# Performance work log

Hardware: AMD Instinct MI355X
Metric: run time of the kernel (lower is better)

Reference implementation:

```python
import jax, jax.numpy as jnp
import numpy as np

N_NODES = 50000
N_EDGES = 800000
IN_DIM = 128
OUT_DIM = 128
N_REL = 8


def setup_inputs() -> dict:
    key = jax.random.key(0)
    k1, k2, k3, k4, k5 = jax.random.split(key, 5)
    x = jax.random.normal(k1, (N_NODES, IN_DIM), dtype=jnp.float32)
    edge_index = jax.random.randint(k2, (2, N_EDGES), 0, N_NODES, dtype=jnp.int32).astype(jnp.int64)
    edge_type = jax.random.randint(k3, (N_EDGES,), 0, N_REL, dtype=jnp.int32).astype(jnp.int64)
    W = jax.random.normal(k4, (N_REL, IN_DIM, OUT_DIM), dtype=jnp.float32) * 0.02
    W0 = jax.random.normal(k5, (IN_DIM, OUT_DIM), dtype=jnp.float32) * 0.02
    return {"x": x, "edge_index": edge_index, "edge_type": edge_type,
            "num_nodes": N_NODES, "W": W, "W0": W0}


def reference(x, edge_index, edge_type, num_nodes, W, W0):
    src = edge_index[0]
    dst = edge_index[1]
    # Per-relation transform of ALL nodes, matching the original loop's x @ W[r].
    xW = jnp.einsum('nd,rdo->rno', x, W)            # [R, N, OUT]
    msgs = xW[edge_type, src]                       # [E, OUT] gather per edge
    agg = jax.ops.segment_sum(msgs, dst, num_segments=num_nodes)  # scatter-add to dst
    out = x @ W0 + agg                              # root/self term
    deg = jax.ops.segment_sum(jnp.ones_like(dst, dtype=out.dtype), dst,
                              num_segments=num_nodes)
    deg = jnp.maximum(deg, 1.0)
    return out / deg[:, None]
```

## Files before the change

kernel.cpp:

```cpp
#include <hip/hip_runtime.h>
#include <hip/hip_bf16.h>
#include <cstdint>
#include <cstddef>


#define NDIM 128
#define NREL 8
#define KCAT 1152
#define COARSE 196
#define EPB 4096

typedef __attribute__((ext_vector_type(8))) short bf16x8;
typedef __attribute__((ext_vector_type(4))) float f32x4;
typedef unsigned int uint32;

__device__ __forceinline__ short f2bf(float f){
  __hip_bfloat16 h = __float2bfloat16(f);
  return *reinterpret_cast<short*>(&h);
}
__device__ __forceinline__ float bfl(uint32 v){ return __uint_as_float(v << 16); }
__device__ __forceinline__ float bfh(uint32 v){ return __uint_as_float(v & 0xFFFF0000u); }

__device__ __forceinline__ void gload_lds16(const void* g, void* l){
  __builtin_amdgcn_global_load_lds(
      (const __attribute__((address_space(1))) unsigned int*)g,
      (__attribute__((address_space(3))) unsigned int*)l, 16, 0, 0);
}

__global__ void k_prep(const float* __restrict__ x, uint32* __restrict__ xb, int n4, int xblocks,
                       const float* __restrict__ W, const float* __restrict__ W0,
                       short* __restrict__ Wb, int wblocks,
                       const int* __restrict__ ei, int* flag, int* coarse_cnt){
  int b = blockIdx.x;
  if (b < xblocks){
    int i = b * 256 + threadIdx.x;
    if (i >= n4) return;
    float4 f = ((const float4*)x)[i];
    uint32 lo = ((uint32)(unsigned short)f2bf(f.x)) | (((uint32)(unsigned short)f2bf(f.y)) << 16);
    uint32 hi = ((uint32)(unsigned short)f2bf(f.z)) | (((uint32)(unsigned short)f2bf(f.w)) << 16);
    ((uint2*)xb)[i] = make_uint2(lo, hi);
  } else if (b < xblocks + wblocks){
    int i = (b - xblocks) * 256 + threadIdx.x;
    if (i >= NDIM * KCAT) return;
    int j  = i / KCAT;
    int t  = i - j * KCAT;
    int r  = t >> 7;
    int kd = t & 127;
    float v = (r < NREL) ? W[(((size_t)r * NDIM + kd) << 7) + j] : W0[((size_t)kd << 7) + j];
    Wb[i] = f2bf(v);
  } else {
    if (threadIdx.x < COARSE) coarse_cnt[threadIdx.x] = 0;
    if (threadIdx.x < 64){
      int v = ei[2 * threadIdx.x + 1];
      unsigned long long m = __ballot(v == 0);
      if (threadIdx.x == 0) flag[0] = (m == ~0ull) ? 1 : 0;
    }
  }
}

__global__ __launch_bounds__(1024) void k_hist(
    const int* __restrict__ ei, const int* __restrict__ et, const int* __restrict__ flag,
    uint32* __restrict__ kv, unsigned char* __restrict__ ctmp,
    int* __restrict__ coarse_cnt, int* __restrict__ blockRes, int E){
  __shared__ int h[COARSE];
  const int b = blockIdx.x;
  for (int i = threadIdx.x; i < COARSE; i += 1024) h[i] = 0;
  __syncthreads();
  const int is64 = flag[0];
  const int e0 = b * EPB;
  for (int i = threadIdx.x; i < EPB; i += 1024){
    int e = e0 + i;
    if (e < E){
      int s, d, t;
      if (is64){ s = ei[2*e]; d = ei[2*(E + e)]; t = et[2*e]; }
      else     { s = ei[e];   d = ei[E + e];     t = et[e];   }
      int c = d >> 8;
      kv[e]   = (uint32)s | ((uint32)t << 16) | ((uint32)(d & 255) << 19);
      ctmp[e] = (unsigned char)c;
      atomicAdd(&h[c], 1);
    }
  }
  __syncthreads();
  for (int c = threadIdx.x; c < COARSE; c += 1024){
    int cnt = h[c];
    int res = 0;
    if (cnt > 0) res = atomicAdd(&coarse_cnt[c], cnt);
    blockRes[b * COARSE + c] = res;
  }
}

__global__ void k_base(const int* __restrict__ coarse_cnt, int* __restrict__ base){
  __shared__ int sm[256];
  int t = threadIdx.x;
  int v = (t < COARSE) ? coarse_cnt[t] : 0;
  sm[t] = v; __syncthreads();
  #pragma unroll
  for (int off = 1; off < 256; off <<= 1){
    int xv = 0; if (t >= off) xv = sm[t - off];
    __syncthreads(); sm[t] += xv; __syncthreads();
  }
  if (t <= COARSE) base[t] = sm[t] - v;
}

__global__ __launch_bounds__(1024) void k_cscatter(
    const uint32* __restrict__ kv, const unsigned char* __restrict__ ctmp,
    const int* __restrict__ base, const int* __restrict__ blockRes,
    uint32* __restrict__ ckv, int E){
  __shared__ int cur[COARSE];
  const int b = blockIdx.x;
  for (int c = threadIdx.x; c < COARSE; c += 1024)
    cur[c] = base[c] + blockRes[b * COARSE + c];
  __syncthreads();
  const int e0 = b * EPB;
  for (int i = threadIdx.x; i < EPB; i += 1024){
    int e = e0 + i;
    if (e < E){
      uint32 v = kv[e];
      int c = ctmp[e];
      int pos = atomicAdd(&cur[c], 1);
      ckv[pos] = v;
    }
  }
}

__global__ __launch_bounds__(1024) void k_fine(
    const uint32* __restrict__ ckv, const int* __restrict__ base,
    uint32* __restrict__ esort, int* __restrict__ rs, int N){
  __shared__ int h[256];
  __shared__ int cur[256];
  const int c  = blockIdx.x;
  const int lo = base[c], hi = base[c + 1];
  const int t  = threadIdx.x;
  if (t < 256) h[t] = 0;
  __syncthreads();
  for (int i = lo + t; i < hi; i += 1024)
    atomicAdd(&h[(ckv[i] >> 19) & 255], 1);
  __syncthreads();
  int v = (t < 256) ? h[t] : 0;
  __syncthreads();
  for (int off = 1; off < 256; off <<= 1){
    int xv = 0;
    if (t < 256 && t >= off) xv = h[t - off];
    __syncthreads();
    if (t < 256) h[t] += xv;
    __syncthreads();
  }
  if (t < 256){
    int excl = h[t] - v;
    cur[t] = lo + excl;
    int idx = c * 256 + t;
    if (idx <= N) rs[idx] = lo + excl;
  }
  __syncthreads();
  for (int i = lo + t; i < hi; i += 1024){
    uint32 v2 = ckv[i];
    int pos = atomicAdd(&cur[(v2 >> 19) & 255], 1);
    esort[pos] = v2;
  }
}

__global__ __launch_bounds__(256) void k_agg(const uint32* __restrict__ xb,
                                             const int* __restrict__ rs,
                                             const uint32* __restrict__ esort,
                                             uint32* __restrict__ hcat,
                                             float* __restrict__ invdeg, int N){
  int wave = threadIdx.x >> 6;
  int lane = threadIdx.x & 63;
  int n = blockIdx.x * 4 + wave;
  if (n >= N) return;
  int beg = rs[n], end = rs[n + 1];
  float2 acc[NREL];
  #pragma unroll
  for (int r = 0; r < NREL; ++r){ acc[r].x = 0.f; acc[r].y = 0.f; }

  int i = beg;
  for (; i + 3 < end; i += 4){
    uint32 p0 = esort[i], p1 = esort[i+1], p2 = esort[i+2], p3 = esort[i+3];
    uint32 v0 = xb[(size_t)(p0 & 0xFFFF) * 64 + lane];
    uint32 v1 = xb[(size_t)(p1 & 0xFFFF) * 64 + lane];
    uint32 v2 = xb[(size_t)(p2 & 0xFFFF) * 64 + lane];
    uint32 v3 = xb[(size_t)(p3 & 0xFFFF) * 64 + lane];
    switch ((p0 >> 16) & 7){
      case 0: acc[0].x+=bfl(v0); acc[0].y+=bfh(v0); break; case 1: acc[1].x+=bfl(v0); acc[1].y+=bfh(v0); break;
      case 2: acc[2].x+=bfl(v0); acc[2].y+=bfh(v0); break; case 3: acc[3].x+=bfl(v0); acc[3].y+=bfh(v0); break;
      case 4: acc[4].x+=bfl(v0); acc[4].y+=bfh(v0); break; case 5: acc[5].x+=bfl(v0); acc[5].y+=bfh(v0); break;
      case 6: acc[6].x+=bfl(v0); acc[6].y+=bfh(v0); break; case 7: acc[7].x+=bfl(v0); acc[7].y+=bfh(v0); break;
    }
    switch ((p1 >> 16) & 7){
      case 0: acc[0].x+=bfl(v1); acc[0].y+=bfh(v1); break; case 1: acc[1].x+=bfl(v1); acc[1].y+=bfh(v1); break;
      case 2: acc[2].x+=bfl(v1); acc[2].y+=bfh(v1); break; case 3: acc[3].x+=bfl(v1); acc[3].y+=bfh(v1); break;
      case 4: acc[4].x+=bfl(v1); acc[4].y+=bfh(v1); break; case 5: acc[5].x+=bfl(v1); acc[5].y+=bfh(v1); break;
      case 6: acc[6].x+=bfl(v1); acc[6].y+=bfh(v1); break; case 7: acc[7].x+=bfl(v1); acc[7].y+=bfh(v1); break;
    }
    switch ((p2 >> 16) & 7){
      case 0: acc[0].x+=bfl(v2); acc[0].y+=bfh(v2); break; case 1: acc[1].x+=bfl(v2); acc[1].y+=bfh(v2); break;
      case 2: acc[2].x+=bfl(v2); acc[2].y+=bfh(v2); break; case 3: acc[3].x+=bfl(v2); acc[3].y+=bfh(v2); break;
      case 4: acc[4].x+=bfl(v2); acc[4].y+=bfh(v2); break; case 5: acc[5].x+=bfl(v2); acc[5].y+=bfh(v2); break;
      case 6: acc[6].x+=bfl(v2); acc[6].y+=bfh(v2); break; case 7: acc[7].x+=bfl(v2); acc[7].y+=bfh(v2); break;
    }
    switch ((p3 >> 16) & 7){
      case 0: acc[0].x+=bfl(v3); acc[0].y+=bfh(v3); break; case 1: acc[1].x+=bfl(v3); acc[1].y+=bfh(v3); break;
      case 2: acc[2].x+=bfl(v3); acc[2].y+=bfh(v3); break; case 3: acc[3].x+=bfl(v3); acc[3].y+=bfh(v3); break;
      case 4: acc[4].x+=bfl(v3); acc[4].y+=bfh(v3); break; case 5: acc[5].x+=bfl(v3); acc[5].y+=bfh(v3); break;
      case 6: acc[6].x+=bfl(v3); acc[6].y+=bfh(v3); break; case 7: acc[7].x+=bfl(v3); acc[7].y+=bfh(v3); break;
    }
  }
  for (; i < end; ++i){
    uint32 p = esort[i];
    uint32 v = xb[(size_t)(p & 0xFFFF) * 64 + lane];
    switch ((p >> 16) & 7){
      case 0: acc[0].x+=bfl(v); acc[0].y+=bfh(v); break; case 1: acc[1].x+=bfl(v); acc[1].y+=bfh(v); break;
      case 2: acc[2].x+=bfl(v); acc[2].y+=bfh(v); break; case 3: acc[3].x+=bfl(v); acc[3].y+=bfh(v); break;
      case 4: acc[4].x+=bfl(v); acc[4].y+=bfh(v); break; case 5: acc[5].x+=bfl(v); acc[5].y+=bfh(v); break;
      case 6: acc[6].x+=bfl(v); acc[6].y+=bfh(v); break; case 7: acc[7].x+=bfl(v); acc[7].y+=bfh(v); break;
    }
  }

  size_t b2 = (size_t)n * (KCAT / 2);
  #pragma unroll
  for (int r = 0; r < NREL; ++r){
    __hip_bfloat162 pk = __float22bfloat162_rn(make_float2(acc[r].x, acc[r].y));
    hcat[b2 + r * 64 + lane] = *reinterpret_cast<uint32*>(&pk);
  }
  hcat[b2 + 512 + lane] = xb[(size_t)n * 64 + lane];
  if (lane == 0){
    int d = end - beg;
    invdeg[n] = 1.0f / (float)(d > 0 ? d : 1);
  }
}

__global__ __launch_bounds__(256) void k_gemm2(
    const short* __restrict__ acat, const short* __restrict__ wb,
    const float* __restrict__ invdeg, float* __restrict__ out, int N)
{
  __shared__ char smem[49152];
  char* As0 = smem;
  char* As1 = smem + 8192;
  char* Bs0 = smem + 16384;
  char* Bs1 = smem + 32768;

  const int tid  = threadIdx.x;
  const int lane = tid & 63;
  const int wid  = tid >> 6;
  const int wr   = wid >> 1;
  const int wc   = wid & 1;
  const int n0   = blockIdx.x * 64;
  const int lr   = lane & 15;
  const int lq   = lane >> 4;

  f32x4 acc[2][4];
  #pragma unroll
  for (int m = 0; m < 2; ++m)
    #pragma unroll
    for (int p = 0; p < 4; ++p)
      acc[m][p] = (f32x4){0.f, 0.f, 0.f, 0.f};

  const int srow = tid >> 3;
  const int scs  = tid & 7;

  auto STAGE = [&](char* Ab, char* Bb, int ks){
    const short* ab = acat + (size_t)n0 * KCAT + ks * 64;
    #pragma unroll
    for (int q = 0; q < 2; ++q){
      int row = q * 32 + srow;
      const short* src = ab + (size_t)row * KCAT + ((scs ^ (row & 7)) << 3);
      gload_lds16(src, Ab + q * 4096 + (wid << 10));
    }
    const short* bb = wb + ks * 64;
    #pragma unroll
    for (int q = 0; q < 4; ++q){
      int j = q * 32 + srow;
      const short* src = bb + (size_t)j * KCAT + ((scs ^ (j & 7)) << 3);
      gload_lds16(src, Bb + q * 4096 + (wid << 10));
    }
  };

  auto COMPUTE = [&](const char* Ab, const char* Bb){
    bf16x8 a[2][2], b[2][4];
    #pragma unroll
    for (int kk = 0; kk < 2; ++kk){
      #pragma unroll
      for (int m = 0; m < 2; ++m){
        int row = wr * 32 + m * 16 + lr;
        int c   = kk * 4 + lq;
        a[kk][m] = *(const bf16x8*)(Ab + row * 128 + ((c ^ (row & 7)) << 4));
      }
      #pragma unroll
      for (int p = 0; p < 4; ++p){
        int j = wc * 64 + p * 16 + lr;
        int c = kk * 4 + lq;
        b[kk][p] = *(const bf16x8*)(Bb + j * 128 + ((c ^ (j & 7)) << 4));
      }
    }
    #pragma unroll
    for (int kk = 0; kk < 2; ++kk)
      #pragma unroll
      for (int m = 0; m < 2; ++m)
        #pragma unroll
        for (int p = 0; p < 4; ++p)
          acc[m][p] = __builtin_amdgcn_mfma_f32_16x16x32_bf16(a[kk][m], b[kk][p], acc[m][p], 0, 0, 0);
  };

  STAGE(As0, Bs0, 0);
  __syncthreads();
  for (int ks = 0; ks < 18; ks += 2){
    STAGE(As1, Bs1, ks + 1);
    COMPUTE(As0, Bs0);
    __syncthreads();
    if (ks + 2 < 18) STAGE(As0, Bs0, ks + 2);
    COMPUTE(As1, Bs1);
    __syncthreads();
  }

  #pragma unroll
  for (int m = 0; m < 2; ++m){
    int rbase = n0 + wr * 32 + m * 16 + lq * 4;
    #pragma unroll
    for (int v = 0; v < 4; ++v){
      int ro = rbase + v;
      if (ro < N){
        float inv = invdeg[ro];
        #pragma unroll
        for (int p = 0; p < 4; ++p)
          out[(((size_t)ro) << 7) + wc * 64 + p * 16 + lr] = acc[m][p][v] * inv;
      }
    }
  }
}

extern "C" void kernel_launch(void* const* d_in, const int* in_sizes, int n_in,
                              void* d_out, int out_size, void* d_ws, size_t ws_size,
                              hipStream_t stream){
  const float* x  = (const float*)d_in[0];
  const int*   ei = (const int*)d_in[1];
  const int*   et = (const int*)d_in[2];
  const float* W  = (const float*)d_in[4];
  const float* W0 = (const float*)d_in[5];
  float* out = (float*)d_out;

  const int N = in_sizes[0] / NDIM;
  const int E = in_sizes[2];
  const int Npad = N + 64;
  const int nblkE = (E + EPB - 1) / EPB;

  char* ws = (char*)d_ws;
  size_t off = 0;
  auto alloc = [&](size_t bytes)->size_t{
    size_t p = off; off = (off + bytes + 255) & ~(size_t)255; return p;
  };
  size_t o_flag = alloc(4);
  size_t o_kv   = alloc((size_t)E * 4);
  size_t o_ct   = alloc((size_t)E);
  size_t o_ckv  = alloc((size_t)E * 4);
  size_t o_es   = alloc((size_t)E * 4);
  size_t o_cc   = alloc(COARSE * 4);
  size_t o_base = alloc((COARSE + 2) * 4);
  size_t o_br   = alloc((size_t)nblkE * COARSE * 4);
  size_t o_rs   = alloc((size_t)(N + 1) * 4);
  size_t o_inv  = alloc((size_t)N * 4);
  size_t o_h    = alloc((size_t)Npad * KCAT * 2);
  size_t o_wb   = alloc((size_t)NDIM * KCAT * 2);
  size_t o_xb   = alloc((size_t)N * NDIM * 2);
  (void)ws_size;

  int*  flag   = (int*)(ws + o_flag);
  uint32* kv   = (uint32*)(ws + o_kv);
  unsigned char* ctmp = (unsigned char*)(ws + o_ct);
  uint32* ckv  = (uint32*)(ws + o_ckv);
  uint32* esort= (uint32*)(ws + o_es);
  int*  ccnt   = (int*)(ws + o_cc);
  int*  base   = (int*)(ws + o_base);
  int*  bres   = (int*)(ws + o_br);
  int*  rs     = (int*)(ws + o_rs);
  float* invdeg= (float*)(ws + o_inv);
  uint32* hcat = (uint32*)(ws + o_h);
  short* acat  = (short*)(ws + o_h);
  short* Wbs   = (short*)(ws + o_wb);
  uint32* xb   = (uint32*)(ws + o_xb);

  const int n4      = N * NDIM / 4;
  const int xblocks = (n4 + 255) / 256;
  const int wblocks = (NDIM * KCAT + 255) / 256;

  k_prep<<<xblocks + wblocks + 1, 256, 0, stream>>>(
      x, xb, n4, xblocks, W, W0, Wbs, wblocks, ei, flag, ccnt);
  k_hist<<<nblkE, 1024, 0, stream>>>(ei, et, flag, kv, ctmp, ccnt, bres, E);
  k_base<<<1, 256, 0, stream>>>(ccnt, base);
  k_cscatter<<<nblkE, 1024, 0, stream>>>(kv, ctmp, base, bres, ckv, E);
  k_fine<<<COARSE, 1024, 0, stream>>>(ckv, base, esort, rs, N);
  k_agg<<<(N + 3) / 4, 256, 0, stream>>>(xb, rs, esort, hcat, invdeg, N);
  k_gemm2<<<(N + 63) / 64, 256, 0, stream>>>(acat, Wbs, invdeg, out, N);
}
```

Measured before the change: 125.9 us.

## Load GEMM weights directly to registers, unroll gather by eight, use nontemporal stores

The GEMM kernel stops staging the weight tile through LDS. Each wave now loads its B fragments straight from global memory into registers, double-buffered across k-steps, which cuts shared memory from 48KB to 16KB and may raise occupancy. The cost is more global/L2 traffic, since waves sharing a column slice each fetch the same weights. The aggregation loop is unrolled by eight to keep more gathers in flight, and the hcat and output writes become nontemporal stores to avoid polluting the cache.

```diff
diff --git a/kernel.cpp b/kernel.cpp
--- a/kernel.cpp
+++ b/kernel.cpp
@@ -159,6 +159,14 @@
   }
 }
 
+#define ACCUM(P, V) \
+  switch (((P) >> 16) & 7){ \
+    case 0: acc[0].x+=bfl(V); acc[0].y+=bfh(V); break; case 1: acc[1].x+=bfl(V); acc[1].y+=bfh(V); break; \
+    case 2: acc[2].x+=bfl(V); acc[2].y+=bfh(V); break; case 3: acc[3].x+=bfl(V); acc[3].y+=bfh(V); break; \
+    case 4: acc[4].x+=bfl(V); acc[4].y+=bfh(V); break; case 5: acc[5].x+=bfl(V); acc[5].y+=bfh(V); break; \
+    case 6: acc[6].x+=bfl(V); acc[6].y+=bfh(V); break; case 7: acc[7].x+=bfl(V); acc[7].y+=bfh(V); break; \
+  }
+
 __global__ __launch_bounds__(256) void k_agg(const uint32* __restrict__ xb,
                                              const int* __restrict__ rs,
                                              const uint32* __restrict__ esort,
@@ -174,55 +182,41 @@
   for (int r = 0; r < NREL; ++r){ acc[r].x = 0.f; acc[r].y = 0.f; }
 
   int i = beg;
+  for (; i + 7 < end; i += 8){
+    uint32 p0 = esort[i],   p1 = esort[i+1], p2 = esort[i+2], p3 = esort[i+3];
+    uint32 p4 = esort[i+4], p5 = esort[i+5], p6 = esort[i+6], p7 = esort[i+7];
+    uint32 v0 = xb[(size_t)(p0 & 0xFFFF) * 64 + lane];
+    uint32 v1 = xb[(size_t)(p1 & 0xFFFF) * 64 + lane];
+    uint32 v2 = xb[(size_t)(p2 & 0xFFFF) * 64 + lane];
+    uint32 v3 = xb[(size_t)(p3 & 0xFFFF) * 64 + lane];
+    uint32 v4 = xb[(size_t)(p4 & 0xFFFF) * 64 + lane];
+    uint32 v5 = xb[(size_t)(p5 & 0xFFFF) * 64 + lane];
+    uint32 v6 = xb[(size_t)(p6 & 0xFFFF) * 64 + lane];
+    uint32 v7 = xb[(size_t)(p7 & 0xFFFF) * 64 + lane];
+    ACCUM(p0, v0) ACCUM(p1, v1) ACCUM(p2, v2) ACCUM(p3, v3)
+    ACCUM(p4, v4) ACCUM(p5, v5) ACCUM(p6, v6) ACCUM(p7, v7)
+  }
   for (; i + 3 < end; i += 4){
     uint32 p0 = esort[i], p1 = esort[i+1], p2 = esort[i+2], p3 = esort[i+3];
     uint32 v0 = xb[(size_t)(p0 & 0xFFFF) * 64 + lane];
     uint32 v1 = xb[(size_t)(p1 & 0xFFFF) * 64 + lane];
     uint32 v2 = xb[(size_t)(p2 & 0xFFFF) * 64 + lane];
     uint32 v3 = xb[(size_t)(p3 & 0xFFFF) * 64 + lane];
-    switch ((p0 >> 16) & 7){
-      case 0: acc[0].x+=bfl(v0); acc[0].y+=bfh(v0); break; case 1: acc[1].x+=bfl(v0); acc[1].y+=bfh(v0); break;
-      case 2: acc[2].x+=bfl(v0); acc[2].y+=bfh(v0); break; case 3: acc[3].x+=bfl(v0); acc[3].y+=bfh(v0); break;
-      case 4: acc[4].x+=bfl(v0); acc[4].y+=bfh(v0); break; case 5: acc[5].x+=bfl(v0); acc[5].y+=bfh(v0); break;
-      case 6: acc[6].x+=bfl(v0); acc[6].y+=bfh(v0); break; case 7: acc[7].x+=bfl(v0); acc[7].y+=bfh(v0); break;
-    }
-    switch ((p1 >> 16) & 7){
-      case 0: acc[0].x+=bfl(v1); acc[0].y+=bfh(v1); break; case 1: acc[1].x+=bfl(v1); acc[1].y+=bfh(v1); break;
-      case 2: acc[2].x+=bfl(v1); acc[2].y+=bfh(v1); break; case 3: acc[3].x+=bfl(v1); acc[3].y+=bfh(v1); break;
-      case 4: acc[4].x+=bfl(v1); acc[4].y+=bfh(v1); break; case 5: acc[5].x+=bfl(v1); acc[5].y+=bfh(v1); break;
-      case 6: acc[6].x+=bfl(v1); acc[6].y+=bfh(v1); break; case 7: acc[7].x+=bfl(v1); acc[7].y+=bfh(v1); break;
-    }
-    switch ((p2 >> 16) & 7){
-      case 0: acc[0].x+=bfl(v2); acc[0].y+=bfh(v2); break; case 1: acc[1].x+=bfl(v2); acc[1].y+=bfh(v2); break;
-      case 2: acc[2].x+=bfl(v2); acc[2].y+=bfh(v2); break; case 3: acc[3].x+=bfl(v2); acc[3].y+=bfh(v2); break;
-      case 4: acc[4].x+=bfl(v2); acc[4].y+=bfh(v2); break; case 5: acc[5].x+=bfl(v2); acc[5].y+=bfh(v2); break;
-      case 6: acc[6].x+=bfl(v2); acc[6].y+=bfh(v2); break; case 7: acc[7].x+=bfl(v2); acc[7].y+=bfh(v2); break;
-    }
-    switch ((p3 >> 16) & 7){
-      case 0: acc[0].x+=bfl(v3); acc[0].y+=bfh(v3); break; case 1: acc[1].x+=bfl(v3); acc[1].y+=bfh(v3); break;
-      case 2: acc[2].x+=bfl(v3); acc[2].y+=bfh(v3); break; case 3: acc[3].x+=bfl(v3); acc[3].y+=bfh(v3); break;
-      case 4: acc[4].x+=bfl(v3); acc[4].y+=bfh(v3); break; case 5: acc[5].x+=bfl(v3); acc[5].y+=bfh(v3); break;
-      case 6: acc[6].x+=bfl(v3); acc[6].y+=bfh(v3); break; case 7: acc[7].x+=bfl(v3); acc[7].y+=bfh(v3); break;
-    }
+    ACCUM(p0, v0) ACCUM(p1, v1) ACCUM(p2, v2) ACCUM(p3, v3)
   }
   for (; i < end; ++i){
     uint32 p = esort[i];
     uint32 v = xb[(size_t)(p & 0xFFFF) * 64 + lane];
-    switch ((p >> 16) & 7){
-      case 0: acc[0].x+=bfl(v); acc[0].y+=bfh(v); break; case 1: acc[1].x+=bfl(v); acc[1].y+=bfh(v); break;
-      case 2: acc[2].x+=bfl(v); acc[2].y+=bfh(v); break; case 3: acc[3].x+=bfl(v); acc[3].y+=bfh(v); break;
-      case 4: acc[4].x+=bfl(v); acc[4].y+=bfh(v); break; case 5: acc[5].x+=bfl(v); acc[5].y+=bfh(v); break;
-      case 6: acc[6].x+=bfl(v); acc[6].y+=bfh(v); break; case 7: acc[7].x+=bfl(v); acc[7].y+=bfh(v); break;
-    }
+    ACCUM(p, v)
   }
 
   size_t b2 = (size_t)n * (KCAT / 2);
   #pragma unroll
   for (int r = 0; r < NREL; ++r){
     __hip_bfloat162 pk = __float22bfloat162_rn(make_float2(acc[r].x, acc[r].y));
-    hcat[b2 + r * 64 + lane] = *reinterpret_cast<uint32*>(&pk);
-  }
-  hcat[b2 + 512 + lane] = xb[(size_t)n * 64 + lane];
+    __builtin_nontemporal_store(*reinterpret_cast<uint32*>(&pk), &hcat[b2 + r * 64 + lane]);
+  }
+  __builtin_nontemporal_store(xb[(size_t)n * 64 + lane], &hcat[b2 + 512 + lane]);
   if (lane == 0){
     int d = end - beg;
     invdeg[n] = 1.0f / (float)(d > 0 ? d : 1);
@@ -230,14 +224,14 @@
 }
 
 __global__ __launch_bounds__(256) void k_gemm2(
-    const short* __restrict__ acat, const short* __restrict__ wb,
-    const float* __restrict__ invdeg, float* __restrict__ out, int N)
+    const short* __restrict__ acat,
+    const short* __restrict__ wb,
+    const float* __restrict__ invdeg,
+    float* __restrict__ out, int N)
 {
-  __shared__ char smem[49152];
+  __shared__ char smem[16384];
   char* As0 = smem;
   char* As1 = smem + 8192;
-  char* Bs0 = smem + 16384;
-  char* Bs1 = smem + 32768;
 
   const int tid  = threadIdx.x;
   const int lane = tid & 63;
@@ -258,7 +252,7 @@
   const int srow = tid >> 3;
   const int scs  = tid & 7;
 
-  auto STAGE = [&](char* Ab, char* Bb, int ks){
+  auto STAGE_A = [&](char* Ab, int ks){
     const short* ab = acat + (size_t)n0 * KCAT + ks * 64;
     #pragma unroll
     for (int q = 0; q < 2; ++q){
@@ -266,32 +260,28 @@
       const short* src = ab + (size_t)row * KCAT + ((scs ^ (row & 7)) << 3);
       gload_lds16(src, Ab + q * 4096 + (wid << 10));
     }
-    const short* bb = wb + ks * 64;
-    #pragma unroll
-    for (int q = 0; q < 4; ++q){
-      int j = q * 32 + srow;
-      const short* src = bb + (size_t)j * KCAT + ((scs ^ (j & 7)) << 3);
-      gload_lds16(src, Bb + q * 4096 + (wid << 10));
-    }
   };
 
-  auto COMPUTE = [&](const char* Ab, const char* Bb){
-    bf16x8 a[2][2], b[2][4];
-    #pragma unroll
-    for (int kk = 0; kk < 2; ++kk){
+  const short* wbase = wb + (size_t)(wc * 64 + lr) * KCAT + lq * 8;
+
+  auto LOAD_B = [&](bf16x8 (&b)[2][4], int ks){
+    #pragma unroll
+    for (int kk = 0; kk < 2; ++kk)
+      #pragma unroll
+      for (int p = 0; p < 4; ++p)
+        b[kk][p] = *(const bf16x8*)(wbase + (size_t)p * 16 * KCAT + ks * 64 + kk * 32);
+  };
+
+  auto COMPUTE = [&](const char* Ab, const bf16x8 (&b)[2][4]){
+    bf16x8 a[2][2];
+    #pragma unroll
+    for (int kk = 0; kk < 2; ++kk)
       #pragma unroll
       for (int m = 0; m < 2; ++m){
         int row = wr * 32 + m * 16 + lr;
         int c   = kk * 4 + lq;
         a[kk][m] = *(const bf16x8*)(Ab + row * 128 + ((c ^ (row & 7)) << 4));
       }
-      #pragma unroll
-      for (int p = 0; p < 4; ++p){
-        int j = wc * 64 + p * 16 + lr;
-        int c = kk * 4 + lq;
-        b[kk][p] = *(const bf16x8*)(Bb + j * 128 + ((c ^ (j & 7)) << 4));
-      }
-    }
     #pragma unroll
     for (int kk = 0; kk < 2; ++kk)
       #pragma unroll
@@ -301,14 +291,20 @@
           acc[m][p] = __builtin_amdgcn_mfma_f32_16x16x32_bf16(a[kk][m], b[kk][p], acc[m][p], 0, 0, 0);
   };
 
-  STAGE(As0, Bs0, 0);
+  bf16x8 bA[2][4], bB[2][4];
+  LOAD_B(bA, 0);
+  STAGE_A(As0, 0);
   __syncthreads();
   for (int ks = 0; ks < 18; ks += 2){
-    STAGE(As1, Bs1, ks + 1);
-    COMPUTE(As0, Bs0);
+    STAGE_A(As1, ks + 1);
+    LOAD_B(bB, ks + 1);
+    COMPUTE(As0, bA);
     __syncthreads();
-    if (ks + 2 < 18) STAGE(As0, Bs0, ks + 2);
-    COMPUTE(As1, Bs1);
+    if (ks + 2 < 18){
+      STAGE_A(As0, ks + 2);
+      LOAD_B(bA, ks + 2);
+    }
+    COMPUTE(As1, bB);
     __syncthreads();
   }
 
@@ -322,7 +318,8 @@
         float inv = invdeg[ro];
         #pragma unroll
         for (int p = 0; p < 4; ++p)
-          out[(((size_t)ro) << 7) + wc * 64 + p * 16 + lr] = acc[m][p][v] * inv;
+          __builtin_nontemporal_store(acc[m][p][v] * inv,
+              &out[(((size_t)ro) << 7) + wc * 64 + p * 16 + lr]);
       }
     }
   }
```

Result: slower. 162.6 us (+29.2%).
